# Kernel tuning notes

Measured on AMD Instinct MI355X. Metric: run time of the kernel, lower is better.

The kernel has to match this reference:

```python
import jax, jax.numpy as jnp
import numpy as np

EMBED_DIM = 1024
NUM_HEADS = 16
HEAD_DIM = EMBED_DIM // NUM_HEADS
WINDOW = 128


def setup_inputs() -> dict:
    key = jax.random.key(0)
    ks = jax.random.split(key, 11)
    B, S, E = 2, 2048, EMBED_DIM
    scale = 1.0 / np.sqrt(E)
    inp = {
        "q": jax.random.normal(ks[0], (B, S, E), jnp.float32),
        "k": jax.random.normal(ks[1], (B, S, E), jnp.float32),
        "v": jax.random.normal(ks[2], (B, S, E), jnp.float32),
        "Wq": jax.random.normal(ks[3], (E, E), jnp.float32) * scale,
        "bq": jnp.zeros((E,), jnp.float32),
        "Wk": jax.random.normal(ks[4], (E, E), jnp.float32) * scale,
        "bk": jnp.zeros((E,), jnp.float32),
        "Wv": jax.random.normal(ks[5], (E, E), jnp.float32) * scale,
        "bv": jnp.zeros((E,), jnp.float32),
        "Wo": jax.random.normal(ks[6], (E, E), jnp.float32) * scale,
        "bo": jnp.zeros((E,), jnp.float32),
    }
    return inp


def reference(q, k, v, Wq, bq, Wk, bk, Wv, bv, Wo, bo):
    B, S, E = q.shape
    H, D = NUM_HEADS, HEAD_DIM
    # projections (torch Linear: x @ W.T + b)
    Q = (q @ Wq.T + bq).reshape(B, S, H, D).transpose(0, 2, 1, 3)  # [B,H,S,D]
    K = (k @ Wk.T + bk).reshape(B, S, H, D).transpose(0, 2, 1, 3)
    V = (v @ Wv.T + bv).reshape(B, S, H, D).transpose(0, 2, 1, 3)
    scores = jnp.einsum("bhqd,bhkd->bhqk", Q, K) / jnp.sqrt(jnp.float32(D))
    idx = jnp.arange(S)
    band = jnp.abs(idx[:, None] - idx[None, :]) <= WINDOW  # [S,S] bool band mask
    scores = jnp.where(band[None, None], scores, -jnp.inf)
    probs = jax.nn.softmax(scores, axis=-1)
    out = jnp.einsum("bhqk,bhkd->bhqd", probs, V)  # [B,H,S,D]
    out = out.transpose(0, 2, 1, 3).reshape(B, S, E)
    return out @ Wo.T + bo
```

## Files before the change

kernel.cpp:

```cpp
#include <hip/hip_runtime.h>
#include <hip/hip_bf16.h>


#define S_LEN 2048
#define EMB   1024
#define NHEAD 16
#define HDIM  64
#define MROWS 4096

typedef __attribute__((ext_vector_type(4))) float f32x4;
typedef __attribute__((ext_vector_type(8))) short bf16x8;

__device__ __forceinline__ unsigned short f2bf(float x){
  union { float f; unsigned u; } un; un.f = x;
  unsigned u = un.u;
  unsigned r = (u + 0x7FFFu + ((u >> 16) & 1u)) >> 16;
  return (unsigned short)r;
}

__device__ __forceinline__ unsigned cvtpk(float lo, float hi){
  __hip_bfloat162 h = __float22bfloat162_rn(make_float2(lo, hi));
  union { __hip_bfloat162 h2; unsigned u; } cv; cv.h2 = h;
  return cv.u;
}

__global__ __launch_bounds__(256) void cvt3_kernel(
    const float4* __restrict__ s0, const float4* __restrict__ s1,
    const float4* __restrict__ s2,
    unsigned long long* __restrict__ d0, unsigned long long* __restrict__ d1,
    unsigned long long* __restrict__ d2)
{
  int i = blockIdx.x * 256 + threadIdx.x;
  const float4* s = (blockIdx.y == 0) ? s0 : (blockIdx.y == 1) ? s1 : s2;
  unsigned long long* d = (blockIdx.y == 0) ? d0 : (blockIdx.y == 1) ? d1 : d2;
  float4 v = s[i];
  d[i] = (unsigned long long)cvtpk(v.x, v.y)
       | ((unsigned long long)cvtpk(v.z, v.w) << 32);
}

__global__ __launch_bounds__(256) void cvt4_kernel(
    const float4* __restrict__ s0, const float4* __restrict__ s1,
    const float4* __restrict__ s2, const float4* __restrict__ s3,
    unsigned long long* __restrict__ d0, unsigned long long* __restrict__ d1,
    unsigned long long* __restrict__ d2, unsigned long long* __restrict__ d3)
{
  int i = blockIdx.x * 256 + threadIdx.x;
  const float4* s = (blockIdx.y == 0) ? s0 : (blockIdx.y == 1) ? s1 :
                    (blockIdx.y == 2) ? s2 : s3;
  unsigned long long* d = (blockIdx.y == 0) ? d0 : (blockIdx.y == 1) ? d1 :
                          (blockIdx.y == 2) ? d2 : d3;
  float4 v = s[i];
  d[i] = (unsigned long long)cvtpk(v.x, v.y)
       | ((unsigned long long)cvtpk(v.z, v.w) << 32);
}

__device__ __forceinline__ void async_copy16(const unsigned short* g, unsigned short* l){
  __builtin_amdgcn_global_load_lds(
      (const __attribute__((address_space(1))) unsigned int*)(const void*)g,
      (__attribute__((address_space(3))) unsigned int*)(void*)l,
      16, 0, 0);
}

__global__ __launch_bounds__(512, 2) void qkv_gemm_kernel(
    const unsigned short* __restrict__ qb, const unsigned short* __restrict__ kb2,
    const unsigned short* __restrict__ vb,
    const unsigned short* __restrict__ Wqb, const unsigned short* __restrict__ Wkb,
    const unsigned short* __restrict__ Wvb,
    const float* __restrict__ bq, const float* __restrict__ bk,
    const float* __restrict__ bv,
    unsigned short* __restrict__ Qp, unsigned short* __restrict__ Kp,
    unsigned short* __restrict__ Vt)
{
  __shared__ __align__(16) unsigned short lds[2][2][256*64];

  const int tid = threadIdx.x, lane = tid & 63, wid = tid >> 6;
  const int wm = wid >> 2, wn = wid & 3;
  const int c = lane & 15, g = lane >> 4;
  const int srow = lane >> 3, sch = lane & 7;

  int bid  = blockIdx.x;
  int bid2 = (bid & 7) * 24 + (bid >> 3);
  const int mx = bid2 & 15, ny = bid2 >> 4;
  const int z  = ny >> 2;
  const int tile_m = mx * 256;
  const int nloc   = (ny & 3) * 256;

  const unsigned short* A = (z == 0) ? qb  : (z == 1) ? kb2 : vb;
  const unsigned short* W = (z == 0) ? Wqb : (z == 1) ? Wkb : Wvb;
  const float*       bias = (z == 0) ? bq  : (z == 1) ? bk  : bv;

  const unsigned short* Asrc = A + (size_t)tile_m * EMB;
  const unsigned short* Bsrc = W + (size_t)nloc * EMB;

  f32x4 acc[8][4] = {};

  auto stageP = [&](int b, int k0, int p){
    int row = wid*32 + p*8 + srow;
    int ch  = sch ^ (row & 7);
    async_copy16(Asrc + (size_t)row*EMB + k0 + ch*8, &lds[b][0][(wid*32 + p*8)*64]);
    async_copy16(Bsrc + (size_t)row*EMB + k0 + ch*8, &lds[b][1][(wid*32 + p*8)*64]);
  };

  stageP(0, 0, 0); stageP(0, 0, 1); stageP(0, 0, 2); stageP(0, 0, 3);

  for (int t = 0; t < 16; ++t){
    const int cb = t & 1, nb = cb ^ 1;
    const bool pre = (t < 15);
    const int k1 = (t + 1) * 64;

    if (pre){
      stageP(nb, k1, 0);
      asm volatile("s_waitcnt vmcnt(2)" ::: "memory");
    } else {
      asm volatile("s_waitcnt vmcnt(0)" ::: "memory");
    }
    asm volatile("s_barrier" ::: "memory");

    bf16x8 bfr[4][2];
#pragma unroll
    for (int ni = 0; ni < 4; ++ni)
#pragma unroll
      for (int kk = 0; kk < 2; ++kk){
        int row = wn*64 + ni*16 + c;
        int ch  = (kk*4 + g) ^ (row & 7);
        bfr[ni][kk] = *(const bf16x8*)&lds[cb][1][row*64 + ch*8];
      }

#pragma unroll
    for (int p = 0; p < 4; ++p){
      bf16x8 af[2][2];
#pragma unroll
      for (int mi = 0; mi < 2; ++mi)
#pragma unroll
        for (int kk = 0; kk < 2; ++kk){
          int row = wm*128 + (p*2 + mi)*16 + c;
          int ch  = (kk*4 + g) ^ (row & 7);
          af[mi][kk] = *(const bf16x8*)&lds[cb][0][row*64 + ch*8];
        }
      if (pre && p < 3) stageP(nb, k1, p + 1);
      __builtin_amdgcn_s_setprio(1);
#pragma unroll
      for (int kk = 0; kk < 2; ++kk)
#pragma unroll
        for (int mi = 0; mi < 2; ++mi)
#pragma unroll
          for (int ni = 0; ni < 4; ++ni)
            acc[p*2 + mi][ni] = __builtin_amdgcn_mfma_f32_16x16x32_bf16(
                af[mi][kk], bfr[ni][kk], acc[p*2 + mi][ni], 0, 0, 0);
      __builtin_amdgcn_s_setprio(0);
    }
    asm volatile("s_barrier" ::: "memory");
  }

  if (z < 2){
    unsigned short* O = (z == 0) ? Qp : Kp;
#pragma unroll
    for (int mf = 0; mf < 8; ++mf){
      int m0 = tile_m + wm*128 + mf*16 + g*4;
      int bb = m0 >> 11, ss = m0 & 2047;
#pragma unroll
      for (int ni = 0; ni < 4; ++ni){
        int nn = nloc + wn*64 + ni*16 + c;
        int h = nn >> 6, d = nn & 63;
        float bvn = bias[nn];
        size_t base = (((size_t)bb*NHEAD + h)*S_LEN + ss)*HDIM + d;
#pragma unroll
        for (int j = 0; j < 4; ++j)
          O[base + (size_t)j*HDIM] = f2bf(acc[mf][ni][j] + bvn);
      }
    }
  } else {
#pragma unroll
    for (int mf = 0; mf < 8; ++mf){
      int m0 = tile_m + wm*128 + mf*16 + g*4;
      int bb = m0 >> 11, ss = m0 & 2047;
      int ssp = (ss & ~31) | (((ss >> 2) & 3) << 3) | (((ss >> 4) & 1) << 2);
#pragma unroll
      for (int ni = 0; ni < 4; ++ni){
        int nn = nloc + wn*64 + ni*16 + c;
        int h = nn >> 6, d = nn & 63;
        float bvn = bias[nn];
        unsigned long long pk =
              (unsigned long long)cvtpk(acc[mf][ni][0] + bvn, acc[mf][ni][1] + bvn)
            | ((unsigned long long)cvtpk(acc[mf][ni][2] + bvn, acc[mf][ni][3] + bvn) << 32);
        *(unsigned long long*)&Vt[(((size_t)bb*NHEAD + h)*HDIM + d)*S_LEN + ssp] = pk;
      }
    }
  }
}

__global__ __launch_bounds__(512) void attn_kernel(
    const unsigned short* __restrict__ Qp, const unsigned short* __restrict__ Kp,
    const unsigned short* __restrict__ Vt, unsigned short* __restrict__ X2)
{
  __shared__ __align__(16) unsigned short Kl[2][64*64];
  __shared__ __align__(16) unsigned short Vl[2][64*64];

  const int tid = threadIdx.x, lane = tid & 63, w = tid >> 6;
  const int c = lane & 15, g = lane >> 4;
  int bid0 = blockIdx.x;
  int bid = (bid0 & 7) * 64 + (bid0 >> 3);
  const int bh = bid >> 4, qc = bid & 15;
  const int qbase = qc * 128;
  const int qw = qbase + w * 16;
  const int qi = qw + c;

  const unsigned short* Kbh = Kp + (size_t)bh * S_LEN * HDIM;
  const unsigned short* Vbh = Vt + (size_t)bh * HDIM * S_LEN;

  const unsigned short* Qb = Qp + ((size_t)bh*S_LEN + qw + c)*HDIM;
  bf16x8 aq0 = *(const bf16x8*)(Qb + g*8);
  bf16x8 aq1 = *(const bf16x8*)(Qb + 32 + g*8);

  f32x4 accO[4] = {};
  float lsum = 0.f;
  const float SC = 0.18033688011112042f;

  int t0 = qbase - 128; if (t0 < 0) t0 = 0;
  int t1 = qbase + 256; if (t1 > S_LEN) t1 = S_LEN;

  const int srow = lane >> 3;
  const int sch  = (lane & 7) ^ srow;

  auto stage = [&](int buf, int kt){
    int r0 = w * 8;
    async_copy16(Kbh + (size_t)(kt + r0 + srow)*HDIM + sch*8, &Kl[buf][r0*64]);
    async_copy16(Vbh + (size_t)(r0 + srow)*S_LEN + kt + sch*8, &Vl[buf][r0*64]);
  };

  auto compute = [&](int buf, int kt){
    f32x4 s[4];
    __builtin_amdgcn_s_setprio(1);
#pragma unroll
    for (int f = 0; f < 4; ++f){
      const unsigned short* Kr = &Kl[buf][(f*16 + c)*64];
      bf16x8 k0 = *(const bf16x8*)(Kr + ((    g) ^ (c & 7))*8);
      bf16x8 k1 = *(const bf16x8*)(Kr + ((4 + g) ^ (c & 7))*8);
      f32x4 a = {0.f, 0.f, 0.f, 0.f};
      a = __builtin_amdgcn_mfma_f32_16x16x32_bf16(k0, aq0, a, 0, 0, 0);
      a = __builtin_amdgcn_mfma_f32_16x16x32_bf16(k1, aq1, a, 0, 0, 0);
      s[f] = a;
    }
    __builtin_amdgcn_s_setprio(0);

    float p[4][4];
    bool nomask = (kt >= qw - 113) && (kt <= qw + 65);
    if (nomask){
#pragma unroll
      for (int f = 0; f < 4; ++f)
#pragma unroll
        for (int j = 0; j < 4; ++j){
          p[f][j] = __builtin_amdgcn_exp2f(s[f][j] * SC);
          lsum += p[f][j];
        }
    } else {
#pragma unroll
      for (int f = 0; f < 4; ++f)
#pragma unroll
        for (int j = 0; j < 4; ++j){
          int dlt = qi - (kt + f*16 + g*4 + j);
          float e = __builtin_amdgcn_exp2f(s[f][j] * SC);
          e = (dlt <= 128 && dlt >= -128) ? e : 0.f;
          p[f][j] = e;
          lsum += e;
        }
    }

    union { unsigned u[4]; bf16x8 v; } A0, A1;
    A0.u[0] = cvtpk(p[0][0], p[0][1]);
    A0.u[1] = cvtpk(p[0][2], p[0][3]);
    A0.u[2] = cvtpk(p[1][0], p[1][1]);
    A0.u[3] = cvtpk(p[1][2], p[1][3]);
    A1.u[0] = cvtpk(p[2][0], p[2][1]);
    A1.u[1] = cvtpk(p[2][2], p[2][3]);
    A1.u[2] = cvtpk(p[3][0], p[3][1]);
    A1.u[3] = cvtpk(p[3][2], p[3][3]);

    __builtin_amdgcn_s_setprio(1);
#pragma unroll
    for (int dblk = 0; dblk < 4; ++dblk){
      const unsigned short* Vr = &Vl[buf][(dblk*16 + c)*64];
      bf16x8 v0 = *(const bf16x8*)(Vr + ((    g) ^ (c & 7))*8);
      bf16x8 v1 = *(const bf16x8*)(Vr + ((4 + g) ^ (c & 7))*8);
      accO[dblk] = __builtin_amdgcn_mfma_f32_16x16x32_bf16(A0.v, v0, accO[dblk], 0, 0, 0);
      accO[dblk] = __builtin_amdgcn_mfma_f32_16x16x32_bf16(A1.v, v1, accO[dblk], 0, 0, 0);
    }
    __builtin_amdgcn_s_setprio(0);
  };

  stage(0, t0);
  int cur = 0;
  for (int kt = t0; kt < t1; kt += 64){
    if (kt + 64 < t1){
      stage(cur ^ 1, kt + 64);
      asm volatile("s_waitcnt vmcnt(2)" ::: "memory");
    } else {
      asm volatile("s_waitcnt vmcnt(0)" ::: "memory");
    }
    asm volatile("s_barrier" ::: "memory");
    bool active = (kt + 63 >= qw - 128) && (kt <= qw + 143);
    if (active) compute(cur, kt);
    asm volatile("s_barrier" ::: "memory");
    cur ^= 1;
  }

  lsum += __shfl_xor(lsum, 16);
  lsum += __shfl_xor(lsum, 32);
  float rl[4];
#pragma unroll
  for (int j = 0; j < 4; ++j)
    rl[j] = 1.f / __shfl(lsum, g*4 + j);

  const int b_ = bh >> 4, h_ = bh & 15;
#pragma unroll
  for (int dblk = 0; dblk < 4; ++dblk)
#pragma unroll
    for (int j = 0; j < 4; ++j){
      int s_ = qw + g*4 + j, d_ = dblk*16 + c;
      X2[((size_t)(b_*S_LEN + s_))*EMB + h_*64 + d_] = f2bf(accO[dblk][j] * rl[j]);
    }
}

__global__ __launch_bounds__(512) void out_gemm_kernel(
    const unsigned short* __restrict__ X2, const unsigned short* __restrict__ Wob,
    const float* __restrict__ bo, float* __restrict__ out)
{
  __shared__ __align__(16) unsigned short lds[4*8192];
  const int tid = threadIdx.x, lane = tid & 63, wid = tid >> 6;
  const int wm = wid >> 2, wn = wid & 3;
  const int c = lane & 15, g = lane >> 4;
  const int srow = lane >> 3, sch = lane & 7;
  const int tile_m = blockIdx.x * 128;
  const int tile_n = blockIdx.y * 128;

  unsigned short* As0 = lds;
  unsigned short* Bs0 = lds + 8192;
  unsigned short* As1 = lds + 16384;
  unsigned short* Bs1 = lds + 24576;

  f32x4 acc[4][2] = {};

  auto stage = [&](unsigned short* As, unsigned short* Bs, int k0){
#pragma unroll
    for (int i = 0; i < 2; ++i){
      int row = (wid*2 + i)*8 + srow;
      int chg = sch ^ (row & 7);
      async_copy16(X2  + (size_t)(tile_m + row)*EMB + k0 + chg*8, As + (wid*2 + i)*512);
      async_copy16(Wob + (size_t)(tile_n + row)*EMB + k0 + chg*8, Bs + (wid*2 + i)*512);
    }
  };

  auto compute = [&](const unsigned short* As, const unsigned short* Bs){
#pragma unroll
    for (int kk = 0; kk < 2; ++kk){
      bf16x8 af[4], bfv[2];
#pragma unroll
      for (int mi = 0; mi < 4; ++mi){
        int row = wm*64 + mi*16 + c;
        int ch  = (kk*4 + g) ^ (row & 7);
        af[mi] = *(const bf16x8*)&As[row*64 + ch*8];
      }
#pragma unroll
      for (int ni = 0; ni < 2; ++ni){
        int row = wn*32 + ni*16 + c;
        int ch  = (kk*4 + g) ^ (row & 7);
        bfv[ni] = *(const bf16x8*)&Bs[row*64 + ch*8];
      }
#pragma unroll
      for (int mi = 0; mi < 4; ++mi)
#pragma unroll
        for (int ni = 0; ni < 2; ++ni)
          acc[mi][ni] = __builtin_amdgcn_mfma_f32_16x16x32_bf16(af[mi], bfv[ni], acc[mi][ni], 0, 0, 0);
    }
  };

  stage(As0, Bs0, 0);
  for (int t = 0; t < 16; ++t){
    const unsigned short* Ac = (t & 1) ? As1 : As0;
    const unsigned short* Bc = (t & 1) ? Bs1 : Bs0;
    unsigned short*       An = (t & 1) ? As0 : As1;
    unsigned short*       Bn = (t & 1) ? Bs0 : Bs1;
    if (t < 15){
      stage(An, Bn, (t + 1) * 64);
      asm volatile("s_waitcnt vmcnt(4)" ::: "memory");
    } else {
      asm volatile("s_waitcnt vmcnt(0)" ::: "memory");
    }
    asm volatile("s_barrier" ::: "memory");
    compute(Ac, Bc);
    asm volatile("s_barrier" ::: "memory");
  }

#pragma unroll
  for (int mi = 0; mi < 4; ++mi){
    int m0 = tile_m + wm*64 + mi*16 + g*4;
#pragma unroll
    for (int ni = 0; ni < 2; ++ni){
      int n = tile_n + wn*32 + ni*16 + c;
      float bvn = bo[n];
#pragma unroll
      for (int j = 0; j < 4; ++j)
        out[(size_t)(m0 + j)*EMB + n] = acc[mi][ni][j] + bvn;
    }
  }
}

extern "C" void kernel_launch(void* const* d_in, const int* in_sizes, int n_in,
                              void* d_out, int out_size, void* d_ws, size_t ws_size,
                              hipStream_t stream)
{
  const float* q  = (const float*)d_in[0];
  const float* k  = (const float*)d_in[1];
  const float* v  = (const float*)d_in[2];
  const float* Wq = (const float*)d_in[3];
  const float* bq = (const float*)d_in[4];
  const float* Wk = (const float*)d_in[5];
  const float* bk = (const float*)d_in[6];
  const float* Wv = (const float*)d_in[7];
  const float* bv = (const float*)d_in[8];
  const float* Wo = (const float*)d_in[9];
  const float* bo = (const float*)d_in[10];
  float* out = (float*)d_out;

  unsigned short* ws = (unsigned short*)d_ws;
  unsigned short* qb  = ws;
  unsigned short* kb  = ws + 4194304;
  unsigned short* vb  = ws + 8388608;
  unsigned short* Wqb = ws + 12582912;
  unsigned short* Wkb = ws + 13631488;
  unsigned short* Wvb = ws + 14680064;
  unsigned short* Wob = ws + 15728640;
  unsigned short* Qp  = ws + 16777216;
  unsigned short* Kp  = ws + 20971520;
  unsigned short* Vt  = ws + 25165824;
  unsigned short* X2  = qb;

  cvt3_kernel<<<dim3(4096, 3), 256, 0, stream>>>(
      (const float4*)q, (const float4*)k, (const float4*)v,
      (unsigned long long*)qb, (unsigned long long*)kb, (unsigned long long*)vb);
  cvt4_kernel<<<dim3(1024, 4), 256, 0, stream>>>(
      (const float4*)Wq, (const float4*)Wk, (const float4*)Wv, (const float4*)Wo,
      (unsigned long long*)Wqb, (unsigned long long*)Wkb,
      (unsigned long long*)Wvb, (unsigned long long*)Wob);

  qkv_gemm_kernel<<<dim3(192), 512, 0, stream>>>(
      qb, kb, vb, Wqb, Wkb, Wvb, bq, bk, bv, Qp, Kp, Vt);

  attn_kernel<<<512, 512, 0, stream>>>(Qp, Kp, Vt, X2);

  out_gemm_kernel<<<dim3(32, 8), 512, 0, stream>>>(X2, Wob, bo, out);
}
```

Measured before the change: 79.17 us.

## Merge conversion kernels and restructure attention into smaller blocks with full K/V preload

The two fp32-to-bf16 conversion launches become a single 7-row grid that skips out-of-range blocks, removing one launch. The attention kernel now uses 64-query blocks of 4 waves (1024 blocks of 256 threads) instead of 128-query blocks of 8 waves. All up to five 64-key K/V tiles are loaded into LDS at once, followed by a single wait and barrier, in place of the double-buffered loop with two barriers per tile. This cuts wasted out-of-band tiles and per-tile synchronisation. In exchange it uses 80KB of LDS per block, which may limit occupancy, and it gives up overlap between loading and compute.

```diff
diff --git a/kernel.cpp b/kernel.cpp
--- a/kernel.cpp
+++ b/kernel.cpp
@@ -24,34 +24,34 @@
   return cv.u;
 }
 
-__global__ __launch_bounds__(256) void cvt3_kernel(
-    const float4* __restrict__ s0, const float4* __restrict__ s1,
-    const float4* __restrict__ s2,
-    unsigned long long* __restrict__ d0, unsigned long long* __restrict__ d1,
-    unsigned long long* __restrict__ d2)
+__global__ __launch_bounds__(256) void cvt7_kernel(
+    const float4* __restrict__ q,  const float4* __restrict__ k,
+    const float4* __restrict__ v,
+    const float4* __restrict__ Wq, const float4* __restrict__ Wk,
+    const float4* __restrict__ Wv, const float4* __restrict__ Wo,
+    unsigned long long* __restrict__ dq, unsigned long long* __restrict__ dk,
+    unsigned long long* __restrict__ dv,
+    unsigned long long* __restrict__ dWq, unsigned long long* __restrict__ dWk,
+    unsigned long long* __restrict__ dWv, unsigned long long* __restrict__ dWo)
 {
   int i = blockIdx.x * 256 + threadIdx.x;
-  const float4* s = (blockIdx.y == 0) ? s0 : (blockIdx.y == 1) ? s1 : s2;
-  unsigned long long* d = (blockIdx.y == 0) ? d0 : (blockIdx.y == 1) ? d1 : d2;
-  float4 v = s[i];
-  d[i] = (unsigned long long)cvtpk(v.x, v.y)
-       | ((unsigned long long)cvtpk(v.z, v.w) << 32);
-}
-
-__global__ __launch_bounds__(256) void cvt4_kernel(
-    const float4* __restrict__ s0, const float4* __restrict__ s1,
-    const float4* __restrict__ s2, const float4* __restrict__ s3,
-    unsigned long long* __restrict__ d0, unsigned long long* __restrict__ d1,
-    unsigned long long* __restrict__ d2, unsigned long long* __restrict__ d3)
-{
-  int i = blockIdx.x * 256 + threadIdx.x;
-  const float4* s = (blockIdx.y == 0) ? s0 : (blockIdx.y == 1) ? s1 :
-                    (blockIdx.y == 2) ? s2 : s3;
-  unsigned long long* d = (blockIdx.y == 0) ? d0 : (blockIdx.y == 1) ? d1 :
-                          (blockIdx.y == 2) ? d2 : d3;
-  float4 v = s[i];
-  d[i] = (unsigned long long)cvtpk(v.x, v.y)
-       | ((unsigned long long)cvtpk(v.z, v.w) << 32);
+  int y = blockIdx.y;
+  const float4* s;
+  unsigned long long* d;
+  int n4;
+  switch (y){
+    case 0: s = q;  d = dq;  n4 = 1048576; break;
+    case 1: s = k;  d = dk;  n4 = 1048576; break;
+    case 2: s = v;  d = dv;  n4 = 1048576; break;
+    case 3: s = Wq; d = dWq; n4 = 262144;  break;
+    case 4: s = Wk; d = dWk; n4 = 262144;  break;
+    case 5: s = Wv; d = dWv; n4 = 262144;  break;
+    default:s = Wo; d = dWo; n4 = 262144;  break;
+  }
+  if (i >= n4) return;
+  float4 x = s[i];
+  d[i] = (unsigned long long)cvtpk(x.x, x.y)
+       | ((unsigned long long)cvtpk(x.z, x.w) << 32);
 }
 
 __device__ __forceinline__ void async_copy16(const unsigned short* g, unsigned short* l){
@@ -189,19 +189,19 @@
   }
 }
 
-__global__ __launch_bounds__(512) void attn_kernel(
+__global__ __launch_bounds__(256) void attn_kernel(
     const unsigned short* __restrict__ Qp, const unsigned short* __restrict__ Kp,
     const unsigned short* __restrict__ Vt, unsigned short* __restrict__ X2)
 {
-  __shared__ __align__(16) unsigned short Kl[2][64*64];
-  __shared__ __align__(16) unsigned short Vl[2][64*64];
+  __shared__ __align__(16) unsigned short Kl[5][64*64];
+  __shared__ __align__(16) unsigned short Vl[5][64*64];
 
   const int tid = threadIdx.x, lane = tid & 63, w = tid >> 6;
   const int c = lane & 15, g = lane >> 4;
   int bid0 = blockIdx.x;
-  int bid = (bid0 & 7) * 64 + (bid0 >> 3);
-  const int bh = bid >> 4, qc = bid & 15;
-  const int qbase = qc * 128;
+  int bid = (bid0 & 7) * 128 + (bid0 >> 3);
+  const int bh = bid >> 5, qt = bid & 31;
+  const int qbase = qt * 64;
   const int qw = qbase + w * 16;
   const int qi = qw + c;
 
@@ -217,23 +217,34 @@
   const float SC = 0.18033688011112042f;
 
   int t0 = qbase - 128; if (t0 < 0) t0 = 0;
-  int t1 = qbase + 256; if (t1 > S_LEN) t1 = S_LEN;
+  int t1 = qbase + 192; if (t1 > S_LEN) t1 = S_LEN;
+  const int nt = (t1 - t0) >> 6;
 
   const int srow = lane >> 3;
   const int sch  = (lane & 7) ^ srow;
 
-  auto stage = [&](int buf, int kt){
-    int r0 = w * 8;
-    async_copy16(Kbh + (size_t)(kt + r0 + srow)*HDIM + sch*8, &Kl[buf][r0*64]);
-    async_copy16(Vbh + (size_t)(r0 + srow)*S_LEN + kt + sch*8, &Vl[buf][r0*64]);
-  };
-
-  auto compute = [&](int buf, int kt){
+  for (int ti = 0; ti < nt; ++ti){
+    int kt = t0 + ti*64;
+#pragma unroll
+    for (int i = 0; i < 2; ++i){
+      int r0 = w*16 + i*8;
+      async_copy16(Kbh + (size_t)(kt + r0 + srow)*HDIM + sch*8, &Kl[ti][r0*64]);
+      async_copy16(Vbh + (size_t)(r0 + srow)*S_LEN + kt + sch*8, &Vl[ti][r0*64]);
+    }
+  }
+  asm volatile("s_waitcnt vmcnt(0)" ::: "memory");
+  asm volatile("s_barrier" ::: "memory");
+
+  for (int ti = 0; ti < nt; ++ti){
+    int kt = t0 + ti*64;
+    bool active = (kt + 63 >= qw - 128) && (kt <= qw + 143);
+    if (!active) continue;
+
     f32x4 s[4];
     __builtin_amdgcn_s_setprio(1);
 #pragma unroll
     for (int f = 0; f < 4; ++f){
-      const unsigned short* Kr = &Kl[buf][(f*16 + c)*64];
+      const unsigned short* Kr = &Kl[ti][(f*16 + c)*64];
       bf16x8 k0 = *(const bf16x8*)(Kr + ((    g) ^ (c & 7))*8);
       bf16x8 k1 = *(const bf16x8*)(Kr + ((4 + g) ^ (c & 7))*8);
       f32x4 a = {0.f, 0.f, 0.f, 0.f};
@@ -279,29 +290,13 @@
     __builtin_amdgcn_s_setprio(1);
 #pragma unroll
     for (int dblk = 0; dblk < 4; ++dblk){
-      const unsigned short* Vr = &Vl[buf][(dblk*16 + c)*64];
+      const unsigned short* Vr = &Vl[ti][(dblk*16 + c)*64];
       bf16x8 v0 = *(const bf16x8*)(Vr + ((    g) ^ (c & 7))*8);
       bf16x8 v1 = *(const bf16x8*)(Vr + ((4 + g) ^ (c & 7))*8);
       accO[dblk] = __builtin_amdgcn_mfma_f32_16x16x32_bf16(A0.v, v0, accO[dblk], 0, 0, 0);
       accO[dblk] = __builtin_amdgcn_mfma_f32_16x16x32_bf16(A1.v, v1, accO[dblk], 0, 0, 0);
     }
     __builtin_amdgcn_s_setprio(0);
-  };
-
-  stage(0, t0);
-  int cur = 0;
-  for (int kt = t0; kt < t1; kt += 64){
-    if (kt + 64 < t1){
-      stage(cur ^ 1, kt + 64);
-      asm volatile("s_waitcnt vmcnt(2)" ::: "memory");
-    } else {
-      asm volatile("s_waitcnt vmcnt(0)" ::: "memory");
-    }
-    asm volatile("s_barrier" ::: "memory");
-    bool active = (kt + 63 >= qw - 128) && (kt <= qw + 143);
-    if (active) compute(cur, kt);
-    asm volatile("s_barrier" ::: "memory");
-    cur ^= 1;
   }
 
   lsum += __shfl_xor(lsum, 16);
@@ -435,18 +430,17 @@
   unsigned short* Vt  = ws + 25165824;
   unsigned short* X2  = qb;
 
-  cvt3_kernel<<<dim3(4096, 3), 256, 0, stream>>>(
+  cvt7_kernel<<<dim3(4096, 7), 256, 0, stream>>>(
       (const float4*)q, (const float4*)k, (const float4*)v,
-      (unsigned long long*)qb, (unsigned long long*)kb, (unsigned long long*)vb);
-  cvt4_kernel<<<dim3(1024, 4), 256, 0, stream>>>(
       (const float4*)Wq, (const float4*)Wk, (const float4*)Wv, (const float4*)Wo,
+      (unsigned long long*)qb, (unsigned long long*)kb, (unsigned long long*)vb,
       (unsigned long long*)Wqb, (unsigned long long*)Wkb,
       (unsigned long long*)Wvb, (unsigned long long*)Wob);
 
   qkv_gemm_kernel<<<dim3(192), 512, 0, stream>>>(
       qb, kb, vb, Wqb, Wkb, Wvb, bq, bk, bv, Qp, Kp, Vt);
 
-  attn_kernel<<<512, 512, 0, stream>>>(Qp, Kp, Vt, X2);
+  attn_kernel<<<1024, 256, 0, stream>>>(Qp, Kp, Vt, X2);
 
   out_gemm_kernel<<<dim3(32, 8), 512, 0, stream>>>(X2, Wob, bo, out);
 }
```

Result: no change. 80.73 us (+2.0%).
